# Kernel optimization log

Measured on AMD Instinct MI355X. Metric: run time of the kernel, lower is better.

Reference implementation:

```python
import jax, jax.numpy as jnp
import numpy as np

B, N, H, E = 32, 8192, 128, 10

def setup_inputs() -> dict:
    key = jax.random.key(0)
    ks = jax.random.split(key, 16)
    nrm = lambda k, s: jax.random.normal(k, s, dtype=jnp.float32) * 0.05
    z = lambda s: jnp.zeros(s, dtype=jnp.float32)
    o = lambda s: jnp.ones(s, dtype=jnp.float32)
    return {
        'points': jax.random.normal(ks[0], (B, N, 3), dtype=jnp.float32),
        'category_ids': jax.random.randint(ks[1], (B,), 0, E, dtype=jnp.int32),
        'pr_w1': nrm(ks[2], (3, H)), 'pr_b1': z((H,)), 'pr_g1': o((H,)), 'pr_be1': z((H,)),
        'pr_w2': nrm(ks[3], (H, H)), 'pr_b2': z((H,)), 'pr_g2': o((H,)), 'pr_be2': z((H,)),
        'cat_emb': nrm(ks[4], (E, H)),
        'cr_w1': nrm(ks[5], (2 * H, H)), 'cr_b1': z((H,)), 'cr_g1': o((H,)), 'cr_be1': z((H,)),
        'cr_w2': nrm(ks[6], (H, H // 2)), 'cr_b2': z((H // 2,)), 'cr_g2': o((H // 2,)), 'cr_be2': z((H // 2,)),
        'cr_w3': nrm(ks[7], (H // 2, 3)), 'cr_b3': z((3,)),
        'sy_w1': nrm(ks[8], (3, H // 2)), 'sy_b1': z((H // 2,)), 'sy_g1': o((H // 2,)), 'sy_be1': z((H // 2,)),
        'sy_w2': nrm(ks[9], (H // 2, 3)), 'sy_b2': z((3,)),
        'sp_w1': nrm(ks[10], (E, 3, H)), 'sp_b1': z((E, H)), 'sp_g1': o((E, H)), 'sp_be1': z((E, H)),
        'sp_w2': nrm(ks[11], (E, H, H // 2)), 'sp_b2': z((E, H // 2)), 'sp_g2': o((E, H // 2)), 'sp_be2': z((E, H // 2)),
        'sp_w3': nrm(ks[12], (E, H // 2, 3)), 'sp_b3': z((E, 3)),
    }

def _ln(x, g, b):
    mu = jnp.mean(x, -1, keepdims=True)
    var = jnp.mean((x - mu) ** 2, -1, keepdims=True)
    return (x - mu) * jax.lax.rsqrt(var + 1e-5) * g + b

def _lrelu(x):
    return jnp.where(x >= 0, x, 0.2 * x)

def reference(points, category_ids,
              pr_w1, pr_b1, pr_g1, pr_be1, pr_w2, pr_b2, pr_g2, pr_be2,
              cat_emb,
              cr_w1, cr_b1, cr_g1, cr_be1, cr_w2, cr_b2, cr_g2, cr_be2, cr_w3, cr_b3,
              sy_w1, sy_b1, sy_g1, sy_be1, sy_w2, sy_b2,
              sp_w1, sp_b1, sp_g1, sp_be1, sp_w2, sp_b2, sp_g2, sp_be2, sp_w3, sp_b3):
    xyz = points[..., :3]
    # shared point refinement MLP
    pf = _lrelu(_ln(points @ pr_w1 + pr_b1, pr_g1, pr_be1))
    pf = _lrelu(_ln(pf @ pr_w2 + pr_b2, pr_g2, pr_be2))  # [B,N,H]
    ce = cat_emb[category_ids][:, None, :]  # [B,1,H]
    comb = jnp.concatenate([pf, jnp.broadcast_to(ce, pf.shape)], axis=-1)  # [B,N,2H]
    h = _lrelu(_ln(comb @ cr_w1 + cr_b1, cr_g1, cr_be1))
    h = _lrelu(_ln(h @ cr_w2 + cr_b2, cr_g2, cr_be2))
    offsets = h @ cr_w3 + cr_b3  # [B,N,3]
    # category-conditioned expert MLPs (MoE dispatch via per-sample gather)
    g = lambda p: p[category_ids]
    ph = jnp.einsum('bni,bio->bno', xyz, g(sp_w1)) + g(sp_b1)[:, None, :]
    ph = _lrelu(_ln(ph, g(sp_g1)[:, None, :], g(sp_be1)[:, None, :]))
    ph = jnp.einsum('bni,bio->bno', ph, g(sp_w2)) + g(sp_b2)[:, None, :]
    ph = _lrelu(_ln(ph, g(sp_g2)[:, None, :], g(sp_be2)[:, None, :]))
    prior = jnp.einsum('bni,bio->bno', ph, g(sp_w3)) + g(sp_b3)[:, None, :]
    offsets = offsets + 0.5 * prior
    # symmetry refinement for categories 2 and 8 (mirror x)
    flip = jnp.array([-1.0, 1.0, 1.0], dtype=points.dtype)
    mx = xyz * flip
    s = _lrelu(_ln(mx @ sy_w1 + sy_b1, sy_g1, sy_be1))
    s = (s @ sy_w2 + sy_b2) * flip
    mask = ((category_ids == 2) | (category_ids == 8))[:, None, None]
    offsets = jnp.where(mask, (offsets + s) * 0.5, offsets)
    return offsets
```

## Files before the change

kernel.cpp:

```cpp
#include <hip/hip_runtime.h>
#include <hip/hip_bf16.h>
#include <stdint.h>

typedef __attribute__((ext_vector_type(8))) short bf16x8;
typedef __attribute__((ext_vector_type(4))) float f32x4;

#define NT 256

#define WS_CE    0
#define WS_PR1   16384
#define WS_PR2   24576
#define WS_CR1   57344
#define WS_CR2   90112
#define WS_CR3   106496
#define WS_SY1   108544
#define WS_SY2   112640
#define WS_SP1   114688
#define WS_SP2   196608
#define WS_SP3   360448


__device__ __forceinline__ short bf1(float x) {
    unsigned u = __float_as_uint(x);
    return (short)((u + 0x7fffu + ((u >> 16) & 1u)) >> 16);
}
__device__ __forceinline__ float bfval(short h) {
    return __uint_as_float(((unsigned)(unsigned short)h) << 16);
}
__device__ __forceinline__ unsigned cvtpk(float lo, float hi) {
    unsigned r;
    asm("v_cvt_pk_bf16_f32 %0, %1, %2" : "=v"(r) : "v"(lo), "v"(hi));
    return r;
}

template<int CTRL>
__device__ __forceinline__ float dpp_add(float v) {
    int o = __builtin_amdgcn_mov_dpp(__float_as_int(v), CTRL, 0xf, 0xf, true);
    return v + __int_as_float(o);
}
__device__ __forceinline__ float row16_sum(float v) {
    v = dpp_add<0x128>(v);
    v = dpp_add<0x124>(v);
    v = dpp_add<0x122>(v);
    v = dpp_add<0x121>(v);
    return v;
}

template<int BYTES>
__device__ __forceinline__ void stage(const char* __restrict__ gsrc, char* ldsdst, int t) {
    const int wu = (t >> 6) << 10;
#pragma unroll
    for (int i = 0; i < BYTES / 4096; ++i)
        __builtin_amdgcn_global_load_lds(
            (const __attribute__((address_space(1))) void*)(gsrc + i * 4096 + t * 16),
            (__attribute__((address_space(3))) void*)(ldsdst + i * 4096 + wu),
            16, 0, 0);
}

template<int NF>
__device__ __forceinline__ void init_acc(f32x4* acc, const float* __restrict__ bias, int c) {
#pragma unroll
    for (int f = 0; f < NF; ++f) {
        const float bv = bias[f * 16 + c];
        acc[f]     = (f32x4){bv, bv, bv, bv};
        acc[8 + f] = (f32x4){bv, bv, bv, bv};
    }
}
__device__ __forceinline__ void init_b3(f32x4& a0, f32x4& a1, const float* __restrict__ b3, int c) {
    const float bv = (c < 3) ? b3[c] : 0.f;
    a0 = (f32x4){bv, bv, bv, bv};
    a1 = (f32x4){bv, bv, bv, bv};
}

__device__ __forceinline__ bf16x8 mkA6(float a0, float a1, float a2, bool active) {
    bf16x8 A = (bf16x8){0, 0, 0, 0, 0, 0, 0, 0};
    if (active) {
        const short h0 = bf1(a0), h1 = bf1(a1), h2 = bf1(a2);
        A[0] = h0; A[1] = h1; A[2] = h2;
        A[3] = bf1(a0 - bfval(h0));
        A[4] = bf1(a1 - bfval(h1));
        A[5] = bf1(a2 - bfval(h2));
    }
    return A;
}

template<int NF>
__device__ __forceinline__ void mfma_reg(bf16x8 A0, bf16x8 A1, const char* __restrict__ Bg,
                                         int lane, f32x4* acc) {
#pragma unroll
    for (int f = 0; f < NF; ++f) {
        bf16x8 B = *(const bf16x8*)(Bg + f * 1024 + lane * 16);
        acc[f]     = __builtin_amdgcn_mfma_f32_16x16x32_bf16(A0, B, acc[f], 0, 0, 0);
        acc[8 + f] = __builtin_amdgcn_mfma_f32_16x16x32_bf16(A1, B, acc[8 + f], 0, 0, 0);
    }
}

template<int NF, int KS>
__device__ __forceinline__ void mfma_staged(const char* actb, char* wb,
                                            const char* __restrict__ Bg,
                                            int R0c, int g, int lane, int t, f32x4* acc) {
    constexpr int CH = NF * 1024;
    const int swz = (R0c & 7) << 4;
    stage<CH>(Bg, wb, t);
    __syncthreads();
#pragma unroll
    for (int ks = 0; ks < KS; ++ks) {
        if (ks + 1 < KS)
            stage<CH>(Bg + (ks + 1) * CH, wb + ((ks + 1) & 1) * 8192, t);
        const char* cur = wb + (ks & 1) * 8192;
        const int kb = ks * 64 + g * 16;
        bf16x8 A0 = *(const bf16x8*)(actb + ((R0c * 256 + kb) ^ swz));
        bf16x8 A1 = *(const bf16x8*)(actb + (((R0c + 16) * 256 + kb) ^ swz));
#pragma unroll
        for (int f = 0; f < NF; ++f) {
            bf16x8 B = *(const bf16x8*)(cur + f * 1024 + lane * 16);
            acc[f]     = __builtin_amdgcn_mfma_f32_16x16x32_bf16(A0, B, acc[f], 0, 0, 0);
            acc[8 + f] = __builtin_amdgcn_mfma_f32_16x16x32_bf16(A1, B, acc[8 + f], 0, 0, 0);
        }
        __syncthreads();
    }
}

__device__ __forceinline__ void mfma3(const char* actb, const char* __restrict__ Bg,
                                      int R0c, int g, int lane, f32x4& a0, f32x4& a1) {
    const int swz = (R0c & 7) << 4;
#pragma unroll
    for (int ks = 0; ks < 2; ++ks) {
        const int kb = ks * 64 + g * 16;
        bf16x8 A0 = *(const bf16x8*)(actb + ((R0c * 256 + kb) ^ swz));
        bf16x8 A1 = *(const bf16x8*)(actb + (((R0c + 16) * 256 + kb) ^ swz));
        bf16x8 B = *(const bf16x8*)(Bg + ks * 1024 + lane * 16);
        a0 = __builtin_amdgcn_mfma_f32_16x16x32_bf16(A0, B, a0, 0, 0, 0);
        a1 = __builtin_amdgcn_mfma_f32_16x16x32_bf16(A1, B, a1, 0, 0, 0);
    }
}

template<int NF>
__device__ __forceinline__ void ln_lrelu_frag(f32x4* acc, int c,
                                              const float* __restrict__ g,
                                              const float* __restrict__ be, float invN) {
    float gv[NF], bev[NF];
#pragma unroll
    for (int f = 0; f < NF; ++f) { gv[f] = g[f * 16 + c]; bev[f] = be[f * 16 + c]; }
#pragma unroll
    for (int rf = 0; rf < 2; ++rf) {
        f32x4 s1 = acc[rf * 8];
        f32x4 s2 = acc[rf * 8] * acc[rf * 8];
#pragma unroll
        for (int f = 1; f < NF; ++f) {
            s1 += acc[rf * 8 + f];
            s2 += acc[rf * 8 + f] * acc[rf * 8 + f];
        }
#pragma unroll
        for (int q = 0; q < 4; ++q) { s1[q] = row16_sum(s1[q]); s2[q] = row16_sum(s2[q]); }
        const f32x4 mu = s1 * invN;
        f32x4 ri;
#pragma unroll
        for (int q = 0; q < 4; ++q)
            ri[q] = rsqrtf(fmaf(s2[q], invN, -mu[q] * mu[q]) + 1e-5f);
#pragma unroll
        for (int f = 0; f < NF; ++f) {
            f32x4 x = (acc[rf * 8 + f] - mu) * ri;
            x = x * gv[f] + bev[f];
            acc[rf * 8 + f] = __builtin_elementwise_max(x, 0.2f * x);
        }
    }
}

template<int NF>
__device__ __forceinline__ void pack_store(char* dst, f32x4* acc, int R0, int c, int g) {
#pragma unroll
    for (int rf = 0; rf < 2; ++rf)
#pragma unroll
        for (int q = 0; q < 4; ++q) {
            const int row = R0 + rf * 16 + g * 4 + q;
            const int rbase = row * 256;
            const int swz = (row & 7) << 4;
#pragma unroll
            for (int m = 0; m < NF / 2; ++m) {
                const unsigned val = cvtpk(acc[rf * 8 + m][q], acc[rf * 8 + m + NF / 2][q]);
                *(unsigned*)(dst + ((rbase + (m * 16 + c) * 4) ^ swz)) = val;
            }
        }
}


__global__ void ce_precompute_kernel(const int* __restrict__ cats,
                                     const float* __restrict__ cat_emb,
                                     const float* __restrict__ cr_w1,
                                     const float* __restrict__ cr_b1,
                                     float* __restrict__ ce_out) {
    const int bb = blockIdx.x;
    const int j = threadIdx.x;
    const int c = cats[bb];
    float acc = cr_b1[j];
#pragma unroll 4
    for (int k = 0; k < 128; ++k)
        acc = fmaf(cat_emb[c * 128 + k], cr_w1[(128 + k) * 128 + j], acc);
    ce_out[bb * 128 + j] = acc;
}

__global__ void wfrag_kernel(
    const float* __restrict__ pr_w1, const float* __restrict__ pr_w2,
    const float* __restrict__ cr_w1, const float* __restrict__ cr_w2,
    const float* __restrict__ cr_w3, const float* __restrict__ sy_w1,
    const float* __restrict__ sy_w2, const float* __restrict__ sp_w1,
    const float* __restrict__ sp_w2, const float* __restrict__ sp_w3,
    char* __restrict__ ws)
{
    const int id = blockIdx.x * 256 + threadIdx.x;
    int local, NF, base, cat = 0;
    const float* W = nullptr;
    int mode;
    int Nstride = 0;

    if (id < 512)        { local = id;          NF = 8; base = WS_PR1; W = pr_w1; mode = 0; Nstride = 128; }
    else if (id < 2560)  { local = id - 512;    NF = 8; base = WS_PR2; W = pr_w2; mode = 1; Nstride = 128; }
    else if (id < 4608)  { local = id - 2560;   NF = 8; base = WS_CR1; W = cr_w1; mode = 1; Nstride = 128; }
    else if (id < 5632)  { local = id - 4608;   NF = 4; base = WS_CR2; W = cr_w2; mode = 1; Nstride = 64; }
    else if (id < 5760)  { local = id - 5632;   NF = 1; base = WS_CR3; W = cr_w3; mode = 2; }
    else if (id < 6016)  { local = id - 5760;   NF = 4; base = WS_SY1; W = sy_w1; mode = 0; Nstride = 64; }
    else if (id < 6144)  { local = id - 6016;   NF = 1; base = WS_SY2; W = sy_w2; mode = 2; }
    else if (id < 11264) { int r = id - 6144;  cat = r / 512;  local = r % 512;
                           NF = 8; base = WS_SP1 + cat * 8192;  W = sp_w1 + cat * 384;  mode = 0; Nstride = 128; }
    else if (id < 21504) { int r = id - 11264; cat = r / 1024; local = r % 1024;
                           NF = 4; base = WS_SP2 + cat * 16384; W = sp_w2 + cat * 8192; mode = 1; Nstride = 64; }
    else                 { int r = id - 21504; cat = r / 128;  local = r % 128;
                           NF = 1; base = WS_SP3 + cat * 2048;  W = sp_w3 + cat * 192;  mode = 2; }

    const int lane = local & 63;
    const int fk = local >> 6;
    const int f = fk % NF;
    const int ks = fk / NF;
    const int c = lane & 15;
    const int g = lane >> 4;
    const int n = f * 16 + c;
    const int p0 = ks * 32 + g * 8;

    bf16x8 H;
#pragma unroll
    for (int e = 0; e < 8; ++e) {
        const int p = p0 + e;
        float v = 0.f;
        if (mode == 0)      { if (p < 6) v = W[(p < 3 ? p : p - 3) * Nstride + n]; }
        else if (mode == 1) { const int k = (p >> 1) + (p & 1) * 64; v = W[k * Nstride + n]; }
        else                { const int k = (p >> 1) + (p & 1) * 32; if (n < 3) v = W[k * 3 + n]; }
        H[e] = bf1(v);
    }
    *(bf16x8*)(ws + base + local * 16) = H;
}


__global__ __launch_bounds__(NT, 3)
void shape_refine_mfma11(
    const float* __restrict__ points, const int* __restrict__ cats,
    const float* __restrict__ pr_b1, const float* __restrict__ pr_g1, const float* __restrict__ pr_be1,
    const float* __restrict__ pr_b2, const float* __restrict__ pr_g2, const float* __restrict__ pr_be2,
    const float* __restrict__ cr_g1, const float* __restrict__ cr_be1,
    const float* __restrict__ cr_b2, const float* __restrict__ cr_g2, const float* __restrict__ cr_be2,
    const float* __restrict__ cr_b3,
    const float* __restrict__ sy_b1, const float* __restrict__ sy_g1, const float* __restrict__ sy_be1,
    const float* __restrict__ sy_b2,
    const float* __restrict__ sp_b1, const float* __restrict__ sp_g1, const float* __restrict__ sp_be1,
    const float* __restrict__ sp_b2, const float* __restrict__ sp_g2, const float* __restrict__ sp_be2,
    const float* __restrict__ sp_b3,
    const char* __restrict__ ws,
    float* __restrict__ out)
{
    __shared__ char act[32768];
    __shared__ char wb[16384];

    const int t = threadIdx.x;
    const int lane = t & 63;
    const int wid = t >> 6;
    const int c = lane & 15;
    const int g = lane >> 4;
    const int R0 = wid * 32;
    const int R0c = R0 + c;

    const int bid = blockIdx.x;
    const int batch = bid >> 6;
    const int pbase = batch * 8192 + (bid & 63) * 128;

    const int cat = __builtin_amdgcn_readfirstlane(cats[batch]);
    const bool sym = (cat == 2) || (cat == 8);

    const float* p0 = points + 3 * (pbase + R0c);
    const float x0 = p0[0], x1 = p0[1], x2 = p0[2];
    const float y0 = p0[48], y1 = p0[49], y2 = p0[50];

    const bf16x8 A0 = mkA6(x0, x1, x2, g == 0);
    const bf16x8 A1 = mkA6(y0, y1, y2, g == 0);

    f32x4 acc[16];
    f32x4 ocr0, ocr1, oo0, oo1;

    init_acc<8>(acc, pr_b1, c);
    mfma_reg<8>(A0, A1, ws + WS_PR1, lane, acc);
    ln_lrelu_frag<8>(acc, c, pr_g1, pr_be1, 1.f / 128.f);
    pack_store<8>(act, acc, R0, c, g);

    init_acc<8>(acc, pr_b2, c);
    mfma_staged<8, 4>(act, wb, ws + WS_PR2, R0c, g, lane, t, acc);
    ln_lrelu_frag<8>(acc, c, pr_g2, pr_be2, 1.f / 128.f);
    pack_store<8>(act, acc, R0, c, g);

    init_acc<8>(acc, (const float*)(ws + WS_CE) + batch * 128, c);
    mfma_staged<8, 4>(act, wb, ws + WS_CR1, R0c, g, lane, t, acc);
    ln_lrelu_frag<8>(acc, c, cr_g1, cr_be1, 1.f / 128.f);
    pack_store<8>(act, acc, R0, c, g);

    init_acc<4>(acc, cr_b2, c);
    mfma_staged<4, 4>(act, wb, ws + WS_CR2, R0c, g, lane, t, acc);
    ln_lrelu_frag<4>(acc, c, cr_g2, cr_be2, 1.f / 64.f);
    pack_store<4>(act, acc, R0, c, g);

    init_b3(ocr0, ocr1, cr_b3, c);
    mfma3(act, ws + WS_CR3, R0c, g, lane, ocr0, ocr1);

    init_acc<8>(acc, sp_b1 + cat * 128, c);
    mfma_reg<8>(A0, A1, ws + WS_SP1 + cat * 8192, lane, acc);
    ln_lrelu_frag<8>(acc, c, sp_g1 + cat * 128, sp_be1 + cat * 128, 1.f / 128.f);
    pack_store<8>(act, acc, R0, c, g);

    init_acc<4>(acc, sp_b2 + cat * 64, c);
    mfma_staged<4, 4>(act, wb, ws + WS_SP2 + cat * 16384, R0c, g, lane, t, acc);
    ln_lrelu_frag<4>(acc, c, sp_g2 + cat * 64, sp_be2 + cat * 64, 1.f / 64.f);
    pack_store<4>(act, acc, R0, c, g);

    init_b3(oo0, oo1, sp_b3 + cat * 3, c);
    mfma3(act, ws + WS_SP3 + cat * 2048, R0c, g, lane, oo0, oo1);
    oo0 = ocr0 + 0.5f * oo0;
    oo1 = ocr1 + 0.5f * oo1;

    if (sym) {
        init_acc<4>(acc, sy_b1, c);
        const bf16x8 S0 = mkA6(-x0, x1, x2, g == 0);
        const bf16x8 S1 = mkA6(-y0, y1, y2, g == 0);
        mfma_reg<4>(S0, S1, ws + WS_SY1, lane, acc);
        ln_lrelu_frag<4>(acc, c, sy_g1, sy_be1, 1.f / 64.f);
        pack_store<4>(act, acc, R0, c, g);
        f32x4 s0, s1;
        init_b3(s0, s1, sy_b2, c);
        mfma3(act, ws + WS_SY2, R0c, g, lane, s0, s1);
        const float flip = (c == 0) ? -1.f : 1.f;
#pragma unroll
        for (int q = 0; q < 4; ++q) {
            oo0[q] = (oo0[q] + flip * s0[q]) * 0.5f;
            oo1[q] = (oo1[q] + flip * s1[q]) * 0.5f;
        }
    }

    if (c < 3) {
#pragma unroll
        for (int q = 0; q < 4; ++q) {
            const int row0 = R0 + g * 4 + q;
            out[3 * (pbase + row0) + c] = oo0[q];
            out[3 * (pbase + row0 + 16) + c] = oo1[q];
        }
    }
}


extern "C" void kernel_launch(void* const* d_in, const int* in_sizes, int n_in,
                              void* d_out, int out_size, void* d_ws, size_t ws_size,
                              hipStream_t stream) {
    const float* points  = (const float*)d_in[0];
    const int*   cats    = (const int*)  d_in[1];
    const float* pr_w1   = (const float*)d_in[2];
    const float* pr_b1   = (const float*)d_in[3];
    const float* pr_g1   = (const float*)d_in[4];
    const float* pr_be1  = (const float*)d_in[5];
    const float* pr_w2   = (const float*)d_in[6];
    const float* pr_b2   = (const float*)d_in[7];
    const float* pr_g2   = (const float*)d_in[8];
    const float* pr_be2  = (const float*)d_in[9];
    const float* cat_emb = (const float*)d_in[10];
    const float* cr_w1   = (const float*)d_in[11];
    const float* cr_b1   = (const float*)d_in[12];
    const float* cr_g1   = (const float*)d_in[13];
    const float* cr_be1  = (const float*)d_in[14];
    const float* cr_w2   = (const float*)d_in[15];
    const float* cr_b2   = (const float*)d_in[16];
    const float* cr_g2   = (const float*)d_in[17];
    const float* cr_be2  = (const float*)d_in[18];
    const float* cr_w3   = (const float*)d_in[19];
    const float* cr_b3   = (const float*)d_in[20];
    const float* sy_w1   = (const float*)d_in[21];
    const float* sy_b1   = (const float*)d_in[22];
    const float* sy_g1   = (const float*)d_in[23];
    const float* sy_be1  = (const float*)d_in[24];
    const float* sy_w2   = (const float*)d_in[25];
    const float* sy_b2   = (const float*)d_in[26];
    const float* sp_w1   = (const float*)d_in[27];
    const float* sp_b1   = (const float*)d_in[28];
    const float* sp_g1   = (const float*)d_in[29];
    const float* sp_be1  = (const float*)d_in[30];
    const float* sp_w2   = (const float*)d_in[31];
    const float* sp_b2   = (const float*)d_in[32];
    const float* sp_g2   = (const float*)d_in[33];
    const float* sp_be2  = (const float*)d_in[34];
    const float* sp_w3   = (const float*)d_in[35];
    const float* sp_b3   = (const float*)d_in[36];

    char* ws = (char*)d_ws;
    float* out = (float*)d_out;

    ce_precompute_kernel<<<dim3(32), dim3(128), 0, stream>>>(cats, cat_emb, cr_w1, cr_b1, (float*)ws);
    wfrag_kernel<<<dim3(89), dim3(256), 0, stream>>>(pr_w1, pr_w2, cr_w1, cr_w2, cr_w3,
                                                     sy_w1, sy_w2, sp_w1, sp_w2, sp_w3, ws);

    shape_refine_mfma11<<<dim3(2048), dim3(NT), 0, stream>>>(
        points, cats,
        pr_b1, pr_g1, pr_be1,
        pr_b2, pr_g2, pr_be2,
        cr_g1, cr_be1,
        cr_b2, cr_g2, cr_be2,
        cr_b3,
        sy_b1, sy_g1, sy_be1, sy_b2,
        sp_b1, sp_g1, sp_be1,
        sp_b2, sp_g2, sp_be2,
        sp_b3,
        ws, out);
}
```

Before: 81.18 us.

## Prefetch next layer weights during LN epilogue and vectorize activation stores

Moves the first weight-chunk staging of each staged GEMM out of mfma_staged and issues it early, so it overlaps the preceding layernorm/activation epilogue (and the first layer's register MFMA). pack_store now writes 8- or 16-byte vector LDS stores instead of several 4-byte stores, and the weight fragment layout for mode 1/2 is permuted to match the new contiguous activation packing. This cuts barrier-exposed global-load latency and LDS store instruction count, but relies on the reordered K permutation staying consistent between wfrag and pack_store.

```diff
diff --git a/kernel.cpp b/kernel.cpp
--- a/kernel.cpp
+++ b/kernel.cpp
@@ -4,6 +4,8 @@
 
 typedef __attribute__((ext_vector_type(8))) short bf16x8;
 typedef __attribute__((ext_vector_type(4))) float f32x4;
+typedef __attribute__((ext_vector_type(4))) unsigned u32x4;
+typedef __attribute__((ext_vector_type(2))) unsigned u32x2;
 
 #define NT 256
 
@@ -101,7 +103,6 @@
                                             int R0c, int g, int lane, int t, f32x4* acc) {
     constexpr int CH = NF * 1024;
     const int swz = (R0c & 7) << 4;
-    stage<CH>(Bg, wb, t);
     __syncthreads();
 #pragma unroll
     for (int ks = 0; ks < KS; ++ks) {
@@ -174,12 +175,19 @@
 #pragma unroll
         for (int q = 0; q < 4; ++q) {
             const int row = R0 + rf * 16 + g * 4 + q;
-            const int rbase = row * 256;
             const int swz = (row & 7) << 4;
-#pragma unroll
-            for (int m = 0; m < NF / 2; ++m) {
-                const unsigned val = cvtpk(acc[rf * 8 + m][q], acc[rf * 8 + m + NF / 2][q]);
-                *(unsigned*)(dst + ((rbase + (m * 16 + c) * 4) ^ swz)) = val;
+            if constexpr (NF == 8) {
+                u32x4 v;
+                v.x = cvtpk(acc[rf * 8 + 0][q], acc[rf * 8 + 4][q]);
+                v.y = cvtpk(acc[rf * 8 + 1][q], acc[rf * 8 + 5][q]);
+                v.z = cvtpk(acc[rf * 8 + 2][q], acc[rf * 8 + 6][q]);
+                v.w = cvtpk(acc[rf * 8 + 3][q], acc[rf * 8 + 7][q]);
+                *(u32x4*)(dst + ((row * 256 + c * 16) ^ swz)) = v;
+            } else {
+                u32x2 v;
+                v.x = cvtpk(acc[rf * 8 + 0][q], acc[rf * 8 + 2][q]);
+                v.y = cvtpk(acc[rf * 8 + 1][q], acc[rf * 8 + 3][q]);
+                *(u32x2*)(dst + ((row * 256 + c * 8) ^ swz)) = v;
             }
         }
 }
@@ -235,16 +243,21 @@
     const int c = lane & 15;
     const int g = lane >> 4;
     const int n = f * 16 + c;
-    const int p0 = ks * 32 + g * 8;
 
     bf16x8 H;
 #pragma unroll
     for (int e = 0; e < 8; ++e) {
-        const int p = p0 + e;
         float v = 0.f;
-        if (mode == 0)      { if (p < 6) v = W[(p < 3 ? p : p - 3) * Nstride + n]; }
-        else if (mode == 1) { const int k = (p >> 1) + (p & 1) * 64; v = W[k * Nstride + n]; }
-        else                { const int k = (p >> 1) + (p & 1) * 32; if (n < 3) v = W[k * 3 + n]; }
+        if (mode == 0) {
+            const int p = ks * 32 + g * 8 + e;
+            if (p < 6) v = W[(p < 3 ? p : p - 3) * Nstride + n];
+        } else if (mode == 1) {
+            const int k = ((e >> 1) + 4 * (e & 1)) * 16 + ks * 4 + g;
+            v = W[k * Nstride + n];
+        } else {
+            const int k = (((e >> 1) & 1) + 2 * (e & 1)) * 16 + ks * 8 + g * 2 + (e >> 2);
+            if (n < 3) v = W[k * 3 + n];
+        }
         H[e] = bf1(v);
     }
     *(bf16x8*)(ws + base + local * 16) = H;
@@ -252,7 +265,7 @@
 
 
 __global__ __launch_bounds__(NT, 3)
-void shape_refine_mfma11(
+void shape_refine_mfma12(
     const float* __restrict__ points, const int* __restrict__ cats,
     const float* __restrict__ pr_b1, const float* __restrict__ pr_g1, const float* __restrict__ pr_be1,
     const float* __restrict__ pr_b2, const float* __restrict__ pr_g2, const float* __restrict__ pr_be2,
@@ -285,6 +298,8 @@
     const int cat = __builtin_amdgcn_readfirstlane(cats[batch]);
     const bool sym = (cat == 2) || (cat == 8);
 
+    stage<8192>(ws + WS_PR2, wb, t);
+
     const float* p0 = points + 3 * (pbase + R0c);
     const float x0 = p0[0], x1 = p0[1], x2 = p0[2];
     const float y0 = p0[48], y1 = p0[49], y2 = p0[50];
@@ -302,16 +317,19 @@
 
     init_acc<8>(acc, pr_b2, c);
     mfma_staged<8, 4>(act, wb, ws + WS_PR2, R0c, g, lane, t, acc);
+    stage<8192>(ws + WS_CR1, wb, t);
     ln_lrelu_frag<8>(acc, c, pr_g2, pr_be2, 1.f / 128.f);
     pack_store<8>(act, acc, R0, c, g);
 
     init_acc<8>(acc, (const float*)(ws + WS_CE) + batch * 128, c);
     mfma_staged<8, 4>(act, wb, ws + WS_CR1, R0c, g, lane, t, acc);
+    stage<4096>(ws + WS_CR2, wb, t);
     ln_lrelu_frag<8>(acc, c, cr_g1, cr_be1, 1.f / 128.f);
     pack_store<8>(act, acc, R0, c, g);
 
     init_acc<4>(acc, cr_b2, c);
     mfma_staged<4, 4>(act, wb, ws + WS_CR2, R0c, g, lane, t, acc);
+    stage<4096>(ws + WS_SP2 + cat * 16384, wb, t);
     ln_lrelu_frag<4>(acc, c, cr_g2, cr_be2, 1.f / 64.f);
     pack_store<4>(act, acc, R0, c, g);
 
@@ -410,7 +428,7 @@
     wfrag_kernel<<<dim3(89), dim3(256), 0, stream>>>(pr_w1, pr_w2, cr_w1, cr_w2, cr_w3,
                                                      sy_w1, sy_w2, sp_w1, sp_w2, sp_w3, ws);
 
-    shape_refine_mfma11<<<dim3(2048), dim3(NT), 0, stream>>>(
+    shape_refine_mfma12<<<dim3(2048), dim3(NT), 0, stream>>>(
         points, cats,
         pr_b1, pr_g1, pr_be1,
         pr_b2, pr_g2, pr_be2,
```

After: 79.16 us. -2.5%, faster.
